# Kernel tuning notes

Measured on AMD Instinct MI355X. Metric: run time of the kernel, lower is better.

Reference implementation:

```python
import jax, jax.numpy as jnp
import numpy as np

B, V, F, P = 32, 256, 128, 64

def setup_inputs() -> dict:
    key = jax.random.key(0)
    k1, k2, k3, k4, k5 = jax.random.split(key, 5)
    q2_obs_scaled = jax.random.uniform(k1, (B, P), dtype=jnp.float32) * 3.0
    amplitude_logits = jax.random.normal(k2, (B, 1, F, P), dtype=jnp.float32)
    volumes = jax.random.uniform(k3, (V, 1), dtype=jnp.float32) + 0.5  # NonNeg, ~median 1
    filters = jax.random.uniform(k4, (1, F), dtype=jnp.float32) * 3.0  # NonNeg q2 positions
    sigma = jax.random.uniform(k5, (), dtype=jnp.float32) * 0.025 + 0.015  # in [0.015, 0.04]
    return {"q2_obs_scaled": q2_obs_scaled, "amplitude_logits": amplitude_logits,
            "volumes": volumes, "filters": filters, "sigma": sigma}

def reference(q2_obs_scaled, amplitude_logits, volumes, filters, sigma):
    # q2_filters: (V,1)*(1,F) -> (V,F) -> (1,V,F,1)
    q2_filters = (volumes * filters)[None, :, :, None]
    # q2_obs_scaled: (B,P) -> (B,1,1,P); difference: (B,V,F,P)
    difference = q2_filters - q2_obs_scaled[:, None, None, :]
    amplitudes = jax.nn.softmax(amplitude_logits, axis=3)  # (B,1,F,P)
    inv = 1.0 / (sigma + 0.001)
    distances = amplitudes * jnp.exp(-0.5 * (difference * inv) ** 2)
    metric = jnp.sum(distances, axis=3)  # (B,V,F)
    return metric
```

## Files before the change

kernel.cpp:

```cpp
#include <hip/hip_runtime.h>

#define B 32
#define V 256
#define F 128
#define P 64

#define LOG2E 1.44269504088896340736f

__global__ __launch_bounds__(256) void extraction_kernel(
    const float* __restrict__ q2,
    const float* __restrict__ logits,
    const float* __restrict__ vol,
    const float* __restrict__ filt,
    const float* __restrict__ sigma_p,
    float* __restrict__ out)
{
    const int bid = blockIdx.x;
    const int b   = bid >> 7;
    const int f   = bid & (F - 1);
    const int tid = threadIdx.x;

    __shared__ float q_s[P];
    __shared__ float amp_s[P];

    if (tid < P) {
        float l = logits[bid * P + tid];
        float m = l;
        #pragma unroll
        for (int off = 32; off > 0; off >>= 1)
            m = fmaxf(m, __shfl_xor(m, off, 64));
        float e = __builtin_amdgcn_exp2f((l - m) * LOG2E);
        float s = e;
        #pragma unroll
        for (int off = 32; off > 0; off >>= 1)
            s += __shfl_xor(s, off, 64);
        amp_s[tid] = e / s;
        q_s[tid]   = q2[b * P + tid];
    }
    __syncthreads();

    const float sig = sigma_p[0];
    const float inv = 1.0f / (sig + 0.001f);
    const float kk  = -0.5f * LOG2E * inv * inv;

    const float x = vol[tid] * filt[f];

    float acc0 = 0.f, acc1 = 0.f, acc2 = 0.f, acc3 = 0.f;
    const float4* q4 = (const float4*)q_s;
    const float4* a4 = (const float4*)amp_s;
    #pragma unroll
    for (int j = 0; j < P / 4; ++j) {
        float4 qv = q4[j];
        float4 av = a4[j];
        float d0 = x - qv.x;
        float d1 = x - qv.y;
        float d2 = x - qv.z;
        float d3 = x - qv.w;
        acc0 += av.x * __builtin_amdgcn_exp2f(kk * d0 * d0);
        acc1 += av.y * __builtin_amdgcn_exp2f(kk * d1 * d1);
        acc2 += av.z * __builtin_amdgcn_exp2f(kk * d2 * d2);
        acc3 += av.w * __builtin_amdgcn_exp2f(kk * d3 * d3);
    }

    out[(b * V + tid) * F + f] = (acc0 + acc1) + (acc2 + acc3);
}

extern "C" void kernel_launch(void* const* d_in, const int* in_sizes, int n_in,
                              void* d_out, int out_size, void* d_ws, size_t ws_size,
                              hipStream_t stream) {
    const float* q2     = (const float*)d_in[0];
    const float* logits = (const float*)d_in[1];
    const float* vol    = (const float*)d_in[2];
    const float* filt   = (const float*)d_in[3];
    const float* sigma  = (const float*)d_in[4];
    float* out = (float*)d_out;

    extraction_kernel<<<B * F, V, 0, stream>>>(q2, logits, vol, filt, sigma, out);
}
```

Measured before the change: 76.09 us.

## Remap threads to filters with per-thread softmax in registers and coalesced stores

Each thread now owns one filter f and computes the 64-wide softmax for (b,f) itself in registers, then loops over several volumes per block. This makes output stores coalesced along F, where the old layout wrote with a stride of F floats. It also removes the shared-memory staging and the barrier. The cost is redundant softmax work (each amplitude row is recomputed by 32 blocks), high register use from two 64-float arrays, and fewer blocks (1024 instead of 4096).

```diff
diff --git a/kernel.cpp b/kernel.cpp
--- a/kernel.cpp
+++ b/kernel.cpp
@@ -4,6 +4,7 @@
 #define V 256
 #define F 128
 #define P 64
+#define VT 8
 
 #define LOG2E 1.44269504088896340736f
 
@@ -16,53 +17,65 @@
     float* __restrict__ out)
 {
     const int bid = blockIdx.x;
-    const int b   = bid >> 7;
-    const int f   = bid & (F - 1);
+    const int b   = bid >> 5;
+    const int v0  = (bid & 31) * VT;
     const int tid = threadIdx.x;
+    const int f   = tid & (F - 1);
+    const int vh  = tid >> 7;
 
-    __shared__ float q_s[P];
-    __shared__ float amp_s[P];
-
-    if (tid < P) {
-        float l = logits[bid * P + tid];
-        float m = l;
-        #pragma unroll
-        for (int off = 32; off > 0; off >>= 1)
-            m = fmaxf(m, __shfl_xor(m, off, 64));
-        float e = __builtin_amdgcn_exp2f((l - m) * LOG2E);
-        float s = e;
-        #pragma unroll
-        for (int off = 32; off > 0; off >>= 1)
-            s += __shfl_xor(s, off, 64);
-        amp_s[tid] = e / s;
-        q_s[tid]   = q2[b * P + tid];
+    float amp[P];
+    const float4* lg4 = (const float4*)(logits + (b * F + f) * P);
+    float m = -3.0e38f;
+    #pragma unroll
+    for (int j = 0; j < P / 4; ++j) {
+        float4 t = lg4[j];
+        amp[4 * j + 0] = t.x;
+        amp[4 * j + 1] = t.y;
+        amp[4 * j + 2] = t.z;
+        amp[4 * j + 3] = t.w;
+        m = fmaxf(m, fmaxf(fmaxf(t.x, t.y), fmaxf(t.z, t.w)));
     }
-    __syncthreads();
+    float sum = 0.f;
+    #pragma unroll
+    for (int p = 0; p < P; ++p) {
+        float e = __builtin_amdgcn_exp2f((amp[p] - m) * LOG2E);
+        amp[p] = e;
+        sum += e;
+    }
+    const float rs = 1.0f / sum;
+    #pragma unroll
+    for (int p = 0; p < P; ++p) amp[p] *= rs;
 
     const float sig = sigma_p[0];
     const float inv = 1.0f / (sig + 0.001f);
-    const float kk  = -0.5f * LOG2E * inv * inv;
+    const float s = sqrtf(0.5f * LOG2E) * inv;
 
-    const float x = vol[tid] * filt[f];
+    float qs[P];
+    #pragma unroll
+    for (int p = 0; p < P; ++p)
+        qs[p] = __uint_as_float(
+            __builtin_amdgcn_readfirstlane(__float_as_uint(q2[b * P + p])));
 
-    float acc0 = 0.f, acc1 = 0.f, acc2 = 0.f, acc3 = 0.f;
-    const float4* q4 = (const float4*)q_s;
-    const float4* a4 = (const float4*)amp_s;
-    #pragma unroll
-    for (int j = 0; j < P / 4; ++j) {
-        float4 qv = q4[j];
-        float4 av = a4[j];
-        float d0 = x - qv.x;
-        float d1 = x - qv.y;
-        float d2 = x - qv.z;
-        float d3 = x - qv.w;
-        acc0 += av.x * __builtin_amdgcn_exp2f(kk * d0 * d0);
-        acc1 += av.y * __builtin_amdgcn_exp2f(kk * d1 * d1);
-        acc2 += av.z * __builtin_amdgcn_exp2f(kk * d2 * d2);
-        acc3 += av.w * __builtin_amdgcn_exp2f(kk * d3 * d3);
+    const float ff = filt[f];
+
+    #pragma unroll 1
+    for (int k = 0; k < VT / 2; ++k) {
+        const int v = v0 + 2 * k + vh;
+        const float x = vol[v] * ff;
+        float a0 = 0.f, a1 = 0.f, a2 = 0.f, a3 = 0.f;
+        #pragma unroll
+        for (int p = 0; p < P; p += 4) {
+            float t0 = (qs[p + 0] - x) * s;
+            float t1 = (qs[p + 1] - x) * s;
+            float t2 = (qs[p + 2] - x) * s;
+            float t3 = (qs[p + 3] - x) * s;
+            a0 += amp[p + 0] * __builtin_amdgcn_exp2f(-(t0 * t0));
+            a1 += amp[p + 1] * __builtin_amdgcn_exp2f(-(t1 * t1));
+            a2 += amp[p + 2] * __builtin_amdgcn_exp2f(-(t2 * t2));
+            a3 += amp[p + 3] * __builtin_amdgcn_exp2f(-(t3 * t3));
+        }
+        out[(b * V + v) * F + f] = (a0 + a1) + (a2 + a3);
     }
-
-    out[(b * V + tid) * F + f] = (acc0 + acc1) + (acc2 + acc3);
 }
 
 extern "C" void kernel_launch(void* const* d_in, const int* in_sizes, int n_in,
@@ -75,5 +88,5 @@
     const float* sigma  = (const float*)d_in[4];
     float* out = (float*)d_out;
 
-    extraction_kernel<<<B * F, V, 0, stream>>>(q2, logits, vol, filt, sigma, out);
+    extraction_kernel<<<B * (V / VT), 256, 0, stream>>>(q2, logits, vol, filt, sigma, out);
 }
```

Result: slower. 78.61 us (+3.3%).
